# Kernel optimization log

Hardware: AMD Instinct MI355X
Metric: run time of the kernel (lower is better)

## Reference

```python
import jax, jax.numpy as jnp
import numpy as np

TOPK = 13
NUM_CLASSES = 80
ALPHA = 1.0
BETA = 6.0
EPS = 1e-9


def _ciou(gt, pd, eps=1e-7):
    """CIoU between gt (B,M,1,4) and pd (B,1,N,4) xyxy boxes -> (B,M,N)."""
    g_x1, g_y1, g_x2, g_y2 = (gt[..., i] for i in range(4))
    p_x1, p_y1, p_x2, p_y2 = (pd[..., i] for i in range(4))
    iw = jnp.clip(jnp.minimum(g_x2, p_x2) - jnp.maximum(g_x1, p_x1), 0.0)
    ih = jnp.clip(jnp.minimum(g_y2, p_y2) - jnp.maximum(g_y1, p_y1), 0.0)
    inter = iw * ih
    w1, h1 = g_x2 - g_x1, g_y2 - g_y1 + eps
    w2, h2 = p_x2 - p_x1, p_y2 - p_y1 + eps
    union = w1 * h1 + w2 * h2 - inter + eps
    iou = inter / union
    cw = jnp.maximum(g_x2, p_x2) - jnp.minimum(g_x1, p_x1)  # enclosing box
    ch = jnp.maximum(g_y2, p_y2) - jnp.minimum(g_y1, p_y1)
    c2 = cw * cw + ch * ch + eps
    rho2 = ((p_x1 + p_x2 - g_x1 - g_x2) ** 2 + (p_y1 + p_y2 - g_y1 - g_y2) ** 2) / 4.0
    v = (4.0 / jnp.pi ** 2) * (jnp.arctan(w2 / h2) - jnp.arctan(w1 / h1)) ** 2
    a = jax.lax.stop_gradient(v / (v - iou + (1.0 + eps)))  # torch.no_grad alpha
    return iou - (rho2 / c2 + v * a)


def setup_inputs() -> dict:
    key = jax.random.key(0)
    ks = jax.random.split(key, 7)
    B, N, M, C = 16, 8400, 32, NUM_CLASSES
    pd_scores = jax.random.uniform(ks[0], (B, N, C), dtype=jnp.float32)
    # YOLO-style anchor centers for 640x640, strides 8/16/32 -> 8400 points
    pts = []
    for s in (8, 16, 32):
        g = 640 // s
        xs = (jnp.arange(g, dtype=jnp.float32) + 0.5) * s
        xx, yy = jnp.meshgrid(xs, xs, indexing="xy")
        pts.append(jnp.stack([xx.ravel(), yy.ravel()], axis=-1))
    anc_points = jnp.concatenate(pts, axis=0)  # (8400, 2)
    ctr = anc_points[None] + jax.random.normal(ks[1], (B, N, 2)) * 8.0
    wh = jax.random.uniform(ks[2], (B, N, 2), minval=8.0, maxval=128.0)
    pd_bboxes = jnp.concatenate([ctr - wh / 2, ctr + wh / 2], axis=-1)
    gctr = jax.random.uniform(ks[3], (B, M, 2), minval=32.0, maxval=608.0)
    gwh = jax.random.uniform(ks[4], (B, M, 2), minval=16.0, maxval=256.0)
    gt_bboxes = jnp.concatenate([gctr - gwh / 2, gctr + gwh / 2], axis=-1)
    gt_labels = jax.random.randint(ks[5], (B, M, 1), 0, C)
    counts = jax.random.randint(ks[6], (B, 1), 1, M + 1)
    mask_gt = (jnp.arange(M)[None, :] < counts)[..., None]  # (B, M, 1) bool prefix-valid
    return {"pd_scores": pd_scores, "pd_bboxes": pd_bboxes, "anc_points": anc_points,
            "gt_labels": gt_labels, "gt_bboxes": gt_bboxes, "mask_gt": mask_gt}


def reference(pd_scores, pd_bboxes, anc_points, gt_labels, gt_bboxes, mask_gt):
    B, N, C = pd_scores.shape
    M = gt_bboxes.shape[1]
    mask_gt2 = mask_gt[..., 0]  # (B, M) bool
    # --- anchors whose centers lie inside each GT box ---
    lt = gt_bboxes[:, :, None, :2]  # (B, M, 1, 2)
    rb = gt_bboxes[:, :, None, 2:]
    anc = anc_points[None, None]    # (1, 1, N, 2)
    deltas = jnp.concatenate([anc - lt, rb - anc], axis=-1)  # (B, M, N, 4)
    mask_in_gts = jnp.min(deltas, axis=-1) > 1e-9            # (B, M, N)
    valid = mask_in_gts & mask_gt2[:, :, None]
    # --- alignment metric = score^alpha * ciou^beta (masked) ---
    cls = gt_labels[..., 0]                      # (B, M)
    scores_t = jnp.swapaxes(pd_scores, 1, 2)     # (B, C, N)
    bbox_scores = jnp.where(valid, scores_t[jnp.arange(B)[:, None], cls], 0.0)  # (B, M, N)
    overlaps = jnp.where(valid, jnp.clip(_ciou(gt_bboxes[:, :, None], pd_bboxes[:, None]), 0.0), 0.0)
    align_metric = bbox_scores ** ALPHA * overlaps ** BETA
    # --- top-k candidate anchors per GT ---
    _, topk_idx = jax.lax.top_k(align_metric, TOPK)          # (B, M, TOPK)
    bi = jnp.arange(B)[:, None, None]
    mi = jnp.arange(M)[None, :, None]
    src = jnp.broadcast_to(mask_gt2[:, :, None], topk_idx.shape)
    mask_topk = jnp.zeros((B, M, N), dtype=bool).at[bi, mi, topk_idx].set(src)
    mask_pos = mask_topk & valid                             # (B, M, N)
    # --- resolve anchors claimed by multiple GTs: keep highest CIoU ---
    fg_count = jnp.sum(mask_pos, axis=1)                     # (B, N)
    best_gt = jnp.argmax(overlaps, axis=1)                   # (B, N)
    is_max = jnp.arange(M)[None, :, None] == best_gt[:, None, :]
    mask_pos_f = jnp.where(fg_count[:, None, :] > 1, is_max, mask_pos).astype(pd_scores.dtype)
    fg_mask = jnp.sum(mask_pos_f, axis=1)                    # (B, N) float 0/1
    target_gt_idx = jnp.argmax(mask_pos_f, axis=1)           # (B, N)
    # --- gather targets ---
    brow = jnp.arange(B)[:, None]
    target_labels = cls[brow, target_gt_idx]                 # (B, N)
    target_bboxes = gt_bboxes[brow, target_gt_idx]           # (B, N, 4)
    target_scores = jax.nn.one_hot(target_labels, C, dtype=jnp.float32) * fg_mask[..., None]
    # --- normalize scores by per-GT best metric/overlap ---
    align_metric = align_metric * mask_pos_f
    pos_align = jnp.max(align_metric, axis=-1, keepdims=True)            # (B, M, 1)
    pos_over = jnp.max(overlaps * mask_pos_f, axis=-1, keepdims=True)    # (B, M, 1)
    norm_align = jnp.max(align_metric * pos_over / (pos_align + EPS), axis=1)  # (B, N)
    target_scores = target_scores * norm_align[..., None]
    return target_labels, target_bboxes, target_scores, fg_mask > 0, target_gt_idx
```

## Files before the change

### kernel.cpp

```cpp
#include <hip/hip_runtime.h>
#include <math.h>

#define B_ 16
#define N_ 8400
#define M_ 32
#define C_ 80
#define TOPK_ 13
#define KL_ 16
#define MAXC_ 2048
#define MZ_ 4
#define MG_ (M_ / MZ_)

__device__ __forceinline__ bool in_gt(double ax, double ay,
    double gx1, double gy1, double gx2, double gy2) {
  return (ax - gx1 > 1e-9) && (ay - gy1 > 1e-9) &&
         (gx2 - ax > 1e-9) && (gy2 - ay > 1e-9);
}

__device__ __forceinline__ double ciou_ov(
    double px1, double py1, double px2, double py2,
    double gx1, double gy1, double gx2, double gy2,
    double atp, double atg) {
  double iw = fmin(gx2, px2) - fmax(gx1, px1); iw = iw > 0.0 ? iw : 0.0;
  double ih = fmin(gy2, py2) - fmax(gy1, py1); ih = ih > 0.0 ? ih : 0.0;
  double inter = iw * ih;
  double w1 = gx2 - gx1, h1 = gy2 - gy1 + 1e-7;
  double w2 = px2 - px1, h2 = py2 - py1 + 1e-7;
  double uni = w1 * h1 + w2 * h2 - inter + 1e-7;
  double iou = inter / uni;
  double cw = fmax(gx2, px2) - fmin(gx1, px1);
  double ch = fmax(gy2, py2) - fmin(gy1, py1);
  double c2 = cw * cw + ch * ch + 1e-7;
  double dx = px1 + px2 - gx1 - gx2, dy = py1 + py2 - gy1 - gy2;
  double rho2 = (dx * dx + dy * dy) * 0.25;
  double dv = atp - atg;
  double v = (4.0 / (M_PI * M_PI)) * dv * dv;
  double a = v / (v - iou + (1.0 + 1e-7));
  double c = iou - (rho2 / c2 + v * a);
  return c > 0.0 ? c : 0.0;
}

#define MERGE_LISTS(av, ai, bv, bi)                                          \
  {                                                                          \
    _Pragma("unroll")                                                        \
    for (int j = 0; j < KL_; ++j) {                                          \
      double vb = bv[KL_ - 1 - j]; int ib = bi[KL_ - 1 - j];                 \
      bool take = (vb > av[j]) || (vb == av[j] && ib < ai[j]);               \
      av[j] = take ? vb : av[j];                                             \
      ai[j] = take ? ib : ai[j];                                             \
    }                                                                        \
    _Pragma("unroll")                                                        \
    for (int dd = 8; dd >= 1; dd >>= 1) {                                    \
      _Pragma("unroll")                                                      \
      for (int j = 0; j < KL_; ++j) {                                        \
        if (!(j & dd)) {                                                     \
          int kk = j | dd;                                                   \
          bool sw = (av[kk] > av[j]) ||                                      \
                    (av[kk] == av[j] && ai[kk] < ai[j]);                     \
          double xv = av[j]; int xi = ai[j];                                 \
          av[j] = sw ? av[kk] : av[j]; ai[j] = sw ? ai[kk] : ai[j];          \
          av[kk] = sw ? xv : av[kk];   ai[kk] = sw ? xi : ai[kk];            \
        }                                                                    \
      }                                                                      \
    }                                                                        \
  }

__global__ __launch_bounds__(256) void k_prep0(
    const float* __restrict__ gt_bboxes, const unsigned char* __restrict__ raw,
    double* __restrict__ atg, unsigned char* __restrict__ mask,
    unsigned int* __restrict__ MPB, unsigned int* __restrict__ CNT,
    unsigned int* __restrict__ PAL, unsigned int* __restrict__ POV) {
  int gid = blockIdx.x * 256 + threadIdx.x;
  if (gid < B_ * N_) MPB[gid] = 0u;
  if (gid < B_ * M_) {
    double x1 = gt_bboxes[gid * 4 + 0], y1 = gt_bboxes[gid * 4 + 1];
    double x2 = gt_bboxes[gid * 4 + 2], y2 = gt_bboxes[gid * 4 + 3];
    atg[gid] = atan((x2 - x1) / (y2 - y1 + 1e-7));
    CNT[gid] = 0u; PAL[gid] = 0u; POV[gid] = 0u;
  }
  if (blockIdx.x == 0) {
    __shared__ int s_bad;
    int t = threadIdx.x;
    if (t == 0) s_bad = 0;
    __syncthreads();
    if (t < B_) {
      int cnt = 0; bool seen0 = false; bool bad = false;
      for (int m = 0; m < M_; ++m) {
        unsigned char v = raw[t * M_ + m];
        if (v > 1) { bad = true; break; }
        if (v) { if (seen0) { bad = true; break; } ++cnt; }
        else seen0 = true;
      }
      if (cnt < 1) bad = true;
      if (bad) atomicOr(&s_bad, 1);
    }
    __syncthreads();
    bool ok = (s_bad == 0);
    const int* ri = (const int*)raw;
    for (int i = t; i < B_ * M_; i += 256)
      mask[i] = ok ? (raw[i] ? 1 : 0) : ((ri[i] != 0) ? 1 : 0);
  }
}

__global__ __launch_bounds__(256) void k_cand(
    const float* __restrict__ pd_scores, const float* __restrict__ pd_bboxes,
    const float* __restrict__ anc, const int* __restrict__ gt_labels,
    const float* __restrict__ gt_bboxes, const unsigned char* __restrict__ mask,
    const double* __restrict__ atg,
    unsigned int* __restrict__ CNT, double* __restrict__ CV,
    int* __restrict__ CI) {
  int b = blockIdx.y, t = threadIdx.x;
  int m0 = blockIdx.z * MG_;
  int n = blockIdx.x * 256 + t;

  __shared__ double s_g[MG_][4];
  __shared__ double s_atg[MG_];
  __shared__ int s_cls[MG_];
  __shared__ unsigned char s_msk[MG_];
  __shared__ int s_any;
  if (t == 0) s_any = 0;
  __syncthreads();
  if (t < MG_) {
    int row = b * M_ + m0 + t;
    unsigned char mk = mask[row];
    s_msk[t] = mk;
    if (mk) atomicOr(&s_any, 1);
    s_g[t][0] = (double)gt_bboxes[row * 4 + 0];
    s_g[t][1] = (double)gt_bboxes[row * 4 + 1];
    s_g[t][2] = (double)gt_bboxes[row * 4 + 2];
    s_g[t][3] = (double)gt_bboxes[row * 4 + 3];
    s_atg[t] = atg[row];
    s_cls[t] = gt_labels[row];
  }
  __syncthreads();
  if (!s_any) return;
  if (n >= N_) return;

  float2 a2 = ((const float2*)anc)[n];
  double ax = (double)a2.x, ay = (double)a2.y;
  bool have = false;
  double px1 = 0, py1 = 0, px2 = 0, py2 = 0, atpn = 0;
  const float* srow = pd_scores + ((size_t)b * N_ + n) * C_;

  for (int mm = 0; mm < MG_; ++mm) {
    if (!s_msk[mm]) continue;
    double gx1 = s_g[mm][0], gy1 = s_g[mm][1], gx2 = s_g[mm][2], gy2 = s_g[mm][3];
    if (!in_gt(ax, ay, gx1, gy1, gx2, gy2)) continue;
    if (!have) {
      float4 pb = ((const float4*)(pd_bboxes + (size_t)b * N_ * 4))[n];
      px1 = (double)pb.x; py1 = (double)pb.y;
      px2 = (double)pb.z; py2 = (double)pb.w;
      atpn = atan((px2 - px1) / ((py2 - py1) + 1e-7));
      have = true;
    }
    double ov = ciou_ov(px1, py1, px2, py2, gx1, gy1, gx2, gy2, atpn, s_atg[mm]);
    double o2 = ov * ov;
    double am = (double)srow[s_cls[mm]] * (o2 * o2 * o2);
    int row = b * M_ + m0 + mm;
    unsigned int idx = atomicAdd(&CNT[row], 1u);
    if (idx < MAXC_) {
      CV[(size_t)row * MAXC_ + idx] = am;
      CI[(size_t)row * MAXC_ + idx] = n;
    }
  }
}

__global__ __launch_bounds__(256) void k_rowsel(
    const double* __restrict__ CV, const int* __restrict__ CI,
    const unsigned int* __restrict__ CNT,
    const float* __restrict__ anc, const float* __restrict__ gt_bboxes,
    const unsigned char* __restrict__ mask, unsigned int* __restrict__ MPB) {
  int row = blockIdx.x;
  if (!mask[row]) return;
  int b = row >> 5, m = row & 31;
  int t = threadIdx.x;
  int cnt = (int)CNT[row]; if (cnt > MAXC_) cnt = MAXC_;
  const double* cv = CV + (size_t)row * MAXC_;
  const int*    ci = CI + (size_t)row * MAXC_;

  double tv[KL_]; int ti[KL_];
#pragma unroll
  for (int j = 0; j < KL_; ++j) { tv[j] = -1.0; ti[j] = 0x7fffffff; }

  for (int i = t; i < cnt; i += 256) {
    double v = cv[i]; int idx = ci[i];
    if (v > tv[TOPK_ - 1] || (v == tv[TOPK_ - 1] && idx < ti[TOPK_ - 1])) {
      double cvv = v; int cii = idx;
#pragma unroll
      for (int j = 0; j < TOPK_; ++j) {
        bool sw = (cvv > tv[j]) || (cvv == tv[j] && cii < ti[j]);
        double xv = tv[j]; int xi = ti[j];
        if (sw) { tv[j] = cvv; ti[j] = cii; cvv = xv; cii = xi; }
      }
    }
  }

#pragma unroll
  for (int d = 1; d <= 32; d <<= 1) {
    double bv[KL_]; int bi[KL_];
#pragma unroll
    for (int j = 0; j < KL_; ++j) {
      bv[j] = __shfl_xor(tv[j], d, 64);
      bi[j] = __shfl_xor(ti[j], d, 64);
    }
    MERGE_LISTS(tv, ti, bv, bi)
  }

  __shared__ double s_v[4 * KL_];
  __shared__ int    s_i[4 * KL_];
  __shared__ int    s_sel[TOPK_];
  __shared__ int    s_p;
  int wave = t >> 6, lane = t & 63;
  if (lane == 0) {
#pragma unroll
    for (int j = 0; j < KL_; ++j) { s_v[wave * KL_ + j] = tv[j]; s_i[wave * KL_ + j] = ti[j]; }
  }
  __syncthreads();
  if (t == 0) {
    double av[KL_]; int ai[KL_];
#pragma unroll
    for (int j = 0; j < KL_; ++j) { av[j] = s_v[j]; ai[j] = s_i[j]; }
    for (int w = 1; w < 4; ++w) {
      double bv[KL_]; int bi[KL_];
#pragma unroll
      for (int j = 0; j < KL_; ++j) { bv[j] = s_v[w * KL_ + j]; bi[j] = s_i[w * KL_ + j]; }
      MERGE_LISTS(av, ai, bv, bi)
    }
    int p = 0;
#pragma unroll
    for (int j = 0; j < TOPK_; ++j)
      if (av[j] > 0.0) s_sel[p++] = ai[j];
    int nn = 0, slot = p;
    while (slot < TOPK_) {
      bool ispos = false;
      for (int q = 0; q < p; ++q) ispos |= (s_sel[q] == nn);
      if (!ispos) s_sel[slot++] = nn | 0x40000000;
      ++nn;
    }
    s_p = p;
  }
  __syncthreads();

  if (t < TOPK_) {
    int e = s_sel[t];
    if (t < s_p) {
      atomicOr(&MPB[(size_t)b * N_ + e], 1u << m);
    } else {
      int n = e & 0x3fffffff;
      double gx1 = gt_bboxes[row * 4 + 0], gy1 = gt_bboxes[row * 4 + 1];
      double gx2 = gt_bboxes[row * 4 + 2], gy2 = gt_bboxes[row * 4 + 3];
      float2 a2 = ((const float2*)anc)[n];
      if (in_gt((double)a2.x, (double)a2.y, gx1, gy1, gx2, gy2))
        atomicOr(&MPB[(size_t)b * N_ + n], 1u << m);
    }
  }
}

__global__ __launch_bounds__(256) void k_colassign(
    const float* __restrict__ pd_scores, const float* __restrict__ pd_bboxes,
    const float* __restrict__ anc, const int* __restrict__ gt_labels,
    const float* __restrict__ gt_bboxes, const unsigned char* __restrict__ mask,
    const double* __restrict__ atg, const unsigned int* __restrict__ MPB,
    unsigned char* __restrict__ TG, unsigned char* __restrict__ FG,
    float* __restrict__ AMC,
    unsigned int* __restrict__ PAL, unsigned int* __restrict__ POV) {
  int b = blockIdx.y;
  int t = threadIdx.x;
  int n = blockIdx.x * 256 + t;
  int lane = t & 63;
  bool act = (n < N_);

  __shared__ double s_g[M_][4];
  __shared__ double s_atg[M_];
  __shared__ int s_cls[M_];
  __shared__ unsigned char s_msk[M_];
  if (t < M_) {
    int gi = b * M_ + t;
    s_g[t][0] = (double)gt_bboxes[gi * 4 + 0];
    s_g[t][1] = (double)gt_bboxes[gi * 4 + 1];
    s_g[t][2] = (double)gt_bboxes[gi * 4 + 2];
    s_g[t][3] = (double)gt_bboxes[gi * 4 + 3];
    s_atg[t] = atg[gi];
    s_cls[t] = gt_labels[gi];
    s_msk[t] = mask[gi];
  }
  __syncthreads();

  size_t i = (size_t)b * N_ + (act ? n : 0);
  unsigned int mpb = act ? MPB[i] : 0u;
  int cnt = __popc(mpb);

  double ax = 0, ay = 0, px1 = 0, py1 = 0, px2 = 0, py2 = 0;
  if (act && cnt >= 1) {
    float2 a2 = ((const float2*)anc)[n];
    float4 pb = ((const float4*)(pd_bboxes + (size_t)b * N_ * 4))[n];
    ax = (double)a2.x; ay = (double)a2.y;
    px1 = (double)pb.x; py1 = (double)pb.y; px2 = (double)pb.z; py2 = (double)pb.w;
  }

  int tg = 0; unsigned char fg = 0; double ov = 0.0;

  if (act && cnt == 1) {
    fg = 1;
    tg = __ffs(mpb) - 1;
    double atpn = atan((px2 - px1) / ((py2 - py1) + 1e-7));
    double g0 = s_g[tg][0], g1 = s_g[tg][1], g2 = s_g[tg][2], g3 = s_g[tg][3];
    bool val = s_msk[tg] && in_gt(ax, ay, g0, g1, g2, g3);
    ov = val ? ciou_ov(px1, py1, px2, py2, g0, g1, g2, g3, atpn, s_atg[tg]) : 0.0;
  }

  unsigned long long flagged = __ballot(act && cnt > 1);
  while (flagged) {
    int src = __ffsll(flagged) - 1;
    flagged &= flagged - 1;
    double qx  = __shfl(ax, src, 64),  qy  = __shfl(ay, src, 64);
    double q1  = __shfl(px1, src, 64), q2  = __shfl(py1, src, 64);
    double q3  = __shfl(px2, src, 64), q4  = __shfl(py2, src, 64);
    double atq = atan((q3 - q1) / ((q4 - q2) + 1e-7));
    int mm = lane & 31;
    double g0 = s_g[mm][0], g1 = s_g[mm][1], g2 = s_g[mm][2], g3 = s_g[mm][3];
    bool val = s_msk[mm] && in_gt(qx, qy, g0, g1, g2, g3);
    double o = val ? ciou_ov(q1, q2, q3, q4, g0, g1, g2, g3, atq, s_atg[mm]) : 0.0;
    int cm = mm;
#pragma unroll
    for (int d = 1; d < 32; d <<= 1) {
      double oo = __shfl_xor(o, d, 64);
      int    om = __shfl_xor(cm, d, 64);
      if (oo > o || (oo == o && om < cm)) { o = oo; cm = om; }
    }
    if (lane == src) { fg = 1; tg = cm; ov = o; }
  }

  if (!act) return;

  TG[i] = (unsigned char)tg;
  FG[i] = fg;
  if (fg) {
    double o2 = ov * ov;
    double am = (double)pd_scores[i * C_ + s_cls[tg]] * (o2 * o2 * o2);
    float ovf = (float)ov, amf = (float)am;
    AMC[i] = amf;
    atomicMax(&PAL[b * M_ + tg], __float_as_uint(amf));
    atomicMax(&POV[b * M_ + tg], __float_as_uint(ovf));
  }
}

__global__ __launch_bounds__(256) void k_emit(
    const int* __restrict__ gt_labels, const float* __restrict__ gt_bboxes,
    const unsigned char* __restrict__ TG, const unsigned char* __restrict__ FG,
    const float* __restrict__ AMC,
    const unsigned int* __restrict__ PAL, const unsigned int* __restrict__ POV,
    float* __restrict__ out) {
  int b = blockIdx.y;
  int n0 = blockIdx.x * 64;
  int t = threadIdx.x;

  __shared__ float s_g[M_][4];
  __shared__ int s_cls[M_];
  __shared__ float s_pal[M_], s_pov[M_];
  __shared__ float s_na[64];
  __shared__ int   s_lab[64];
  __shared__ int   s_tg[64];
  __shared__ unsigned char s_fg[64];
  if (t < M_) {
    int gi = b * M_ + t;
    s_g[t][0] = gt_bboxes[gi * 4 + 0];
    s_g[t][1] = gt_bboxes[gi * 4 + 1];
    s_g[t][2] = gt_bboxes[gi * 4 + 2];
    s_g[t][3] = gt_bboxes[gi * 4 + 3];
    s_cls[t] = gt_labels[gi];
    s_pal[t] = __uint_as_float(PAL[gi]);
    s_pov[t] = __uint_as_float(POV[gi]);
  }
  __syncthreads();

  if (t < 64) {
    int n = n0 + t;
    if (n < N_) {
      size_t i = (size_t)b * N_ + n;
      int tg = TG[i];
      unsigned char fg = FG[i];
      float na = 0.0f;
      if (fg) {
        double am = (double)AMC[i];
        na = (float)(am * (double)s_pov[tg] / ((double)s_pal[tg] + 1e-9));
      }
      s_na[t] = na; s_lab[t] = s_cls[tg]; s_tg[t] = tg; s_fg[t] = fg;
    }
  }
  __syncthreads();

  float* o0 = out;
  float* o1 = out + (size_t)B_ * N_;
  float* o2 = out + (size_t)B_ * N_ * 5;
  float* o3 = out + (size_t)B_ * N_ * 85;
  float* o4 = out + (size_t)B_ * N_ * 86;

  if (t < 64) {
    int n = n0 + t;
    if (n < N_) {
      size_t i = (size_t)b * N_ + n;
      o0[i] = (float)s_lab[t];
      o3[i] = s_fg[t] ? 1.0f : 0.0f;
      o4[i] = (float)s_tg[t];
      int tg = s_tg[t];
      ((float4*)o1)[i] = make_float4(s_g[tg][0], s_g[tg][1], s_g[tg][2], s_g[tg][3]);
    }
  }

#pragma unroll
  for (int k = 0; k < 5; ++k) {
    int id = t + k * 256;
    int a = id / 20, j = id % 20;
    int n = n0 + a;
    if (n < N_) {
      int lab = s_lab[a];
      float na = s_fg[a] ? s_na[a] : 0.0f;
      int c0 = 4 * j;
      float4 w;
      w.x = (c0 + 0 == lab) ? na : 0.0f;
      w.y = (c0 + 1 == lab) ? na : 0.0f;
      w.z = (c0 + 2 == lab) ? na : 0.0f;
      w.w = (c0 + 3 == lab) ? na : 0.0f;
      ((float4*)(o2 + ((size_t)b * N_ + n) * C_))[j] = w;
    }
  }
}

extern "C" void kernel_launch(void* const* d_in, const int* in_sizes, int n_in,
                              void* d_out, int out_size, void* d_ws, size_t ws_size,
                              hipStream_t stream) {
  const float* pd_scores = (const float*)d_in[0];
  const float* pd_bboxes = (const float*)d_in[1];
  const float* anc       = (const float*)d_in[2];
  const int*   gt_labels = (const int*)d_in[3];
  const float* gt_bboxes = (const float*)d_in[4];
  const unsigned char* mask_raw = (const unsigned char*)d_in[5];

  char* ws = (char*)d_ws;
  size_t off = 0;
  double* CV  = (double*)(ws + off); off += (size_t)B_ * M_ * MAXC_ * 8;
  double* ATG = (double*)(ws + off); off += (size_t)B_ * M_ * 8;
  int*    CI  = (int*)(ws + off);    off += (size_t)B_ * M_ * MAXC_ * 4;
  unsigned int* MPB = (unsigned int*)(ws + off); off += (size_t)B_ * N_ * 4;
  unsigned int* CNT = (unsigned int*)(ws + off); off += (size_t)B_ * M_ * 4;
  unsigned int* PAL = (unsigned int*)(ws + off); off += (size_t)B_ * M_ * 4;
  unsigned int* POV = (unsigned int*)(ws + off); off += (size_t)B_ * M_ * 4;
  unsigned char* TG   = (unsigned char*)(ws + off); off += (size_t)B_ * N_;
  unsigned char* FG   = (unsigned char*)(ws + off); off += (size_t)B_ * N_;
  float* AMC = (float*)(ws + off); off += (size_t)B_ * N_ * 4;
  unsigned char* MASK = (unsigned char*)(ws + off); off += (size_t)B_ * M_;

  k_prep0<<<(B_ * N_ + 255) / 256, 256, 0, stream>>>(gt_bboxes, mask_raw, ATG,
                                                     MASK, MPB, CNT, PAL, POV);
  dim3 gc((N_ + 255) / 256, B_, MZ_);
  k_cand<<<gc, 256, 0, stream>>>(pd_scores, pd_bboxes, anc, gt_labels,
                                 gt_bboxes, MASK, ATG, CNT, CV, CI);
  k_rowsel<<<B_ * M_, 256, 0, stream>>>(CV, CI, CNT, anc, gt_bboxes, MASK, MPB);
  dim3 gbn((N_ + 255) / 256, B_);
  k_colassign<<<gbn, 256, 0, stream>>>(pd_scores, pd_bboxes, anc, gt_labels,
                                       gt_bboxes, MASK, ATG, MPB,
                                       TG, FG, AMC, PAL, POV);
  dim3 gem((N_ + 63) / 64, B_);
  k_emit<<<gem, 256, 0, stream>>>(gt_labels, gt_bboxes, TG, FG, AMC, PAL, POV,
                                  (float*)d_out);
}
```

Baseline: 162.5 us.

## Shrink prep kernel, recompute atan in place, wave-per-row topk, emit outputs in colassign

The prep kernel shrinks to two blocks. The MPB zeroing moves into the candidate kernel, and the per-GT atan is recomputed in shared-memory setup instead of being stored to a workspace array. Row top-k selection now uses one wavefront per GT row with four rows per block, which removes the cross-wave shared-memory merge and the barriers. Label, bbox, fg and index outputs are written directly in the column-assign kernel, so the final kernel only writes the score tensor. Together these cut the size of the prep launch, workspace traffic and block synchronisation. The costs are redundant atan work per block and a single wave scanning each candidate list.

```diff
diff --git a/kernel.cpp b/kernel.cpp
--- a/kernel.cpp
+++ b/kernel.cpp
@@ -66,18 +66,11 @@
   }
 
 __global__ __launch_bounds__(256) void k_prep0(
-    const float* __restrict__ gt_bboxes, const unsigned char* __restrict__ raw,
-    double* __restrict__ atg, unsigned char* __restrict__ mask,
-    unsigned int* __restrict__ MPB, unsigned int* __restrict__ CNT,
+    const unsigned char* __restrict__ raw, unsigned char* __restrict__ mask,
+    unsigned int* __restrict__ CNT,
     unsigned int* __restrict__ PAL, unsigned int* __restrict__ POV) {
   int gid = blockIdx.x * 256 + threadIdx.x;
-  if (gid < B_ * N_) MPB[gid] = 0u;
-  if (gid < B_ * M_) {
-    double x1 = gt_bboxes[gid * 4 + 0], y1 = gt_bboxes[gid * 4 + 1];
-    double x2 = gt_bboxes[gid * 4 + 2], y2 = gt_bboxes[gid * 4 + 3];
-    atg[gid] = atan((x2 - x1) / (y2 - y1 + 1e-7));
-    CNT[gid] = 0u; PAL[gid] = 0u; POV[gid] = 0u;
-  }
+  if (gid < B_ * M_) { CNT[gid] = 0u; PAL[gid] = 0u; POV[gid] = 0u; }
   if (blockIdx.x == 0) {
     __shared__ int s_bad;
     int t = threadIdx.x;
@@ -106,12 +99,14 @@
     const float* __restrict__ pd_scores, const float* __restrict__ pd_bboxes,
     const float* __restrict__ anc, const int* __restrict__ gt_labels,
     const float* __restrict__ gt_bboxes, const unsigned char* __restrict__ mask,
-    const double* __restrict__ atg,
+    unsigned int* __restrict__ MPB,
     unsigned int* __restrict__ CNT, double* __restrict__ CV,
     int* __restrict__ CI) {
   int b = blockIdx.y, t = threadIdx.x;
   int m0 = blockIdx.z * MG_;
   int n = blockIdx.x * 256 + t;
+
+  if (blockIdx.z == 0 && n < N_) MPB[(size_t)b * N_ + n] = 0u;
 
   __shared__ double s_g[MG_][4];
   __shared__ double s_atg[MG_];
@@ -125,11 +120,10 @@
     unsigned char mk = mask[row];
     s_msk[t] = mk;
     if (mk) atomicOr(&s_any, 1);
-    s_g[t][0] = (double)gt_bboxes[row * 4 + 0];
-    s_g[t][1] = (double)gt_bboxes[row * 4 + 1];
-    s_g[t][2] = (double)gt_bboxes[row * 4 + 2];
-    s_g[t][3] = (double)gt_bboxes[row * 4 + 3];
-    s_atg[t] = atg[row];
+    double x1 = (double)gt_bboxes[row * 4 + 0], y1 = (double)gt_bboxes[row * 4 + 1];
+    double x2 = (double)gt_bboxes[row * 4 + 2], y2 = (double)gt_bboxes[row * 4 + 3];
+    s_g[t][0] = x1; s_g[t][1] = y1; s_g[t][2] = x2; s_g[t][3] = y2;
+    s_atg[t] = atan((x2 - x1) / (y2 - y1 + 1e-7));
     s_cls[t] = gt_labels[row];
   }
   __syncthreads();
@@ -170,10 +164,11 @@
     const unsigned int* __restrict__ CNT,
     const float* __restrict__ anc, const float* __restrict__ gt_bboxes,
     const unsigned char* __restrict__ mask, unsigned int* __restrict__ MPB) {
-  int row = blockIdx.x;
-  if (!mask[row]) return;
+  int t = threadIdx.x;
+  int lane = t & 63;
+  int row = blockIdx.x * 4 + (t >> 6);
+  if (row >= B_ * M_ || !mask[row]) return;
   int b = row >> 5, m = row & 31;
-  int t = threadIdx.x;
   int cnt = (int)CNT[row]; if (cnt > MAXC_) cnt = MAXC_;
   const double* cv = CV + (size_t)row * MAXC_;
   const int*    ci = CI + (size_t)row * MAXC_;
@@ -182,7 +177,7 @@
 #pragma unroll
   for (int j = 0; j < KL_; ++j) { tv[j] = -1.0; ti[j] = 0x7fffffff; }
 
-  for (int i = t; i < cnt; i += 256) {
+  for (int i = lane; i < cnt; i += 64) {
     double v = cv[i]; int idx = ci[i];
     if (v > tv[TOPK_ - 1] || (v == tv[TOPK_ - 1] && idx < ti[TOPK_ - 1])) {
       double cvv = v; int cii = idx;
@@ -206,47 +201,38 @@
     MERGE_LISTS(tv, ti, bv, bi)
   }
 
-  __shared__ double s_v[4 * KL_];
-  __shared__ int    s_i[4 * KL_];
-  __shared__ int    s_sel[TOPK_];
-  __shared__ int    s_p;
-  int wave = t >> 6, lane = t & 63;
+  int sel[TOPK_]; int p = 0;
   if (lane == 0) {
 #pragma unroll
-    for (int j = 0; j < KL_; ++j) { s_v[wave * KL_ + j] = tv[j]; s_i[wave * KL_ + j] = ti[j]; }
-  }
-  __syncthreads();
-  if (t == 0) {
-    double av[KL_]; int ai[KL_];
-#pragma unroll
-    for (int j = 0; j < KL_; ++j) { av[j] = s_v[j]; ai[j] = s_i[j]; }
-    for (int w = 1; w < 4; ++w) {
-      double bv[KL_]; int bi[KL_];
-#pragma unroll
-      for (int j = 0; j < KL_; ++j) { bv[j] = s_v[w * KL_ + j]; bi[j] = s_i[w * KL_ + j]; }
-      MERGE_LISTS(av, ai, bv, bi)
-    }
-    int p = 0;
+    for (int j = 0; j < TOPK_; ++j) sel[j] = -1;
 #pragma unroll
     for (int j = 0; j < TOPK_; ++j)
-      if (av[j] > 0.0) s_sel[p++] = ai[j];
+      if (tv[j] > 0.0) sel[p++] = ti[j];
     int nn = 0, slot = p;
     while (slot < TOPK_) {
       bool ispos = false;
-      for (int q = 0; q < p; ++q) ispos |= (s_sel[q] == nn);
-      if (!ispos) s_sel[slot++] = nn | 0x40000000;
+#pragma unroll
+      for (int q = 0; q < TOPK_; ++q) ispos |= (q < p && sel[q] == nn);
+      if (!ispos) { 
+#pragma unroll
+        for (int q = 0; q < TOPK_; ++q) if (q == slot) sel[q] = nn | 0x40000000;
+        ++slot;
+      }
       ++nn;
     }
-    s_p = p;
-  }
-  __syncthreads();
-
-  if (t < TOPK_) {
-    int e = s_sel[t];
-    if (t < s_p) {
-      atomicOr(&MPB[(size_t)b * N_ + e], 1u << m);
+  }
+  int pbc = __shfl(p, 0, 64);
+  int mine = -1;
+#pragma unroll
+  for (int j = 0; j < TOPK_; ++j) {
+    int v = __shfl(sel[j], 0, 64);
+    if (lane == j) mine = v;
+  }
+  if (lane < TOPK_) {
+    if (lane < pbc) {
+      atomicOr(&MPB[(size_t)b * N_ + mine], 1u << m);
     } else {
-      int n = e & 0x3fffffff;
+      int n = mine & 0x3fffffff;
       double gx1 = gt_bboxes[row * 4 + 0], gy1 = gt_bboxes[row * 4 + 1];
       double gx2 = gt_bboxes[row * 4 + 2], gy2 = gt_bboxes[row * 4 + 3];
       float2 a2 = ((const float2*)anc)[n];
@@ -260,10 +246,11 @@
     const float* __restrict__ pd_scores, const float* __restrict__ pd_bboxes,
     const float* __restrict__ anc, const int* __restrict__ gt_labels,
     const float* __restrict__ gt_bboxes, const unsigned char* __restrict__ mask,
-    const double* __restrict__ atg, const unsigned int* __restrict__ MPB,
+    const unsigned int* __restrict__ MPB,
     unsigned char* __restrict__ TG, unsigned char* __restrict__ FG,
     float* __restrict__ AMC,
-    unsigned int* __restrict__ PAL, unsigned int* __restrict__ POV) {
+    unsigned int* __restrict__ PAL, unsigned int* __restrict__ POV,
+    float* __restrict__ out) {
   int b = blockIdx.y;
   int t = threadIdx.x;
   int n = blockIdx.x * 256 + t;
@@ -276,11 +263,10 @@
   __shared__ unsigned char s_msk[M_];
   if (t < M_) {
     int gi = b * M_ + t;
-    s_g[t][0] = (double)gt_bboxes[gi * 4 + 0];
-    s_g[t][1] = (double)gt_bboxes[gi * 4 + 1];
-    s_g[t][2] = (double)gt_bboxes[gi * 4 + 2];
-    s_g[t][3] = (double)gt_bboxes[gi * 4 + 3];
-    s_atg[t] = atg[gi];
+    double x1 = (double)gt_bboxes[gi * 4 + 0], y1 = (double)gt_bboxes[gi * 4 + 1];
+    double x2 = (double)gt_bboxes[gi * 4 + 2], y2 = (double)gt_bboxes[gi * 4 + 3];
+    s_g[t][0] = x1; s_g[t][1] = y1; s_g[t][2] = x2; s_g[t][3] = y2;
+    s_atg[t] = atan((x2 - x1) / (y2 - y1 + 1e-7));
     s_cls[t] = gt_labels[gi];
     s_msk[t] = mask[gi];
   }
@@ -343,10 +329,20 @@
     atomicMax(&PAL[b * M_ + tg], __float_as_uint(amf));
     atomicMax(&POV[b * M_ + tg], __float_as_uint(ovf));
   }
-}
-
-__global__ __launch_bounds__(256) void k_emit(
-    const int* __restrict__ gt_labels, const float* __restrict__ gt_bboxes,
+
+  float* o0 = out;
+  float* o1 = out + (size_t)B_ * N_;
+  float* o3 = out + (size_t)B_ * N_ * 85;
+  float* o4 = out + (size_t)B_ * N_ * 86;
+  o0[i] = (float)s_cls[tg];
+  o3[i] = fg ? 1.0f : 0.0f;
+  o4[i] = (float)tg;
+  ((float4*)o1)[i] = make_float4((float)s_g[tg][0], (float)s_g[tg][1],
+                                 (float)s_g[tg][2], (float)s_g[tg][3]);
+}
+
+__global__ __launch_bounds__(256) void k_sc(
+    const int* __restrict__ gt_labels,
     const unsigned char* __restrict__ TG, const unsigned char* __restrict__ FG,
     const float* __restrict__ AMC,
     const unsigned int* __restrict__ PAL, const unsigned int* __restrict__ POV,
@@ -355,19 +351,12 @@
   int n0 = blockIdx.x * 64;
   int t = threadIdx.x;
 
-  __shared__ float s_g[M_][4];
   __shared__ int s_cls[M_];
   __shared__ float s_pal[M_], s_pov[M_];
   __shared__ float s_na[64];
   __shared__ int   s_lab[64];
-  __shared__ int   s_tg[64];
-  __shared__ unsigned char s_fg[64];
   if (t < M_) {
     int gi = b * M_ + t;
-    s_g[t][0] = gt_bboxes[gi * 4 + 0];
-    s_g[t][1] = gt_bboxes[gi * 4 + 1];
-    s_g[t][2] = gt_bboxes[gi * 4 + 2];
-    s_g[t][3] = gt_bboxes[gi * 4 + 3];
     s_cls[t] = gt_labels[gi];
     s_pal[t] = __uint_as_float(PAL[gi]);
     s_pov[t] = __uint_as_float(POV[gi]);
@@ -379,35 +368,17 @@
     if (n < N_) {
       size_t i = (size_t)b * N_ + n;
       int tg = TG[i];
-      unsigned char fg = FG[i];
       float na = 0.0f;
-      if (fg) {
+      if (FG[i]) {
         double am = (double)AMC[i];
         na = (float)(am * (double)s_pov[tg] / ((double)s_pal[tg] + 1e-9));
       }
-      s_na[t] = na; s_lab[t] = s_cls[tg]; s_tg[t] = tg; s_fg[t] = fg;
+      s_na[t] = na; s_lab[t] = s_cls[tg];
     }
   }
   __syncthreads();
 
-  float* o0 = out;
-  float* o1 = out + (size_t)B_ * N_;
   float* o2 = out + (size_t)B_ * N_ * 5;
-  float* o3 = out + (size_t)B_ * N_ * 85;
-  float* o4 = out + (size_t)B_ * N_ * 86;
-
-  if (t < 64) {
-    int n = n0 + t;
-    if (n < N_) {
-      size_t i = (size_t)b * N_ + n;
-      o0[i] = (float)s_lab[t];
-      o3[i] = s_fg[t] ? 1.0f : 0.0f;
-      o4[i] = (float)s_tg[t];
-      int tg = s_tg[t];
-      ((float4*)o1)[i] = make_float4(s_g[tg][0], s_g[tg][1], s_g[tg][2], s_g[tg][3]);
-    }
-  }
-
 #pragma unroll
   for (int k = 0; k < 5; ++k) {
     int id = t + k * 256;
@@ -415,7 +386,7 @@
     int n = n0 + a;
     if (n < N_) {
       int lab = s_lab[a];
-      float na = s_fg[a] ? s_na[a] : 0.0f;
+      float na = s_na[a];
       int c0 = 4 * j;
       float4 w;
       w.x = (c0 + 0 == lab) ? na : 0.0f;
@@ -440,7 +411,6 @@
   char* ws = (char*)d_ws;
   size_t off = 0;
   double* CV  = (double*)(ws + off); off += (size_t)B_ * M_ * MAXC_ * 8;
-  double* ATG = (double*)(ws + off); off += (size_t)B_ * M_ * 8;
   int*    CI  = (int*)(ws + off);    off += (size_t)B_ * M_ * MAXC_ * 4;
   unsigned int* MPB = (unsigned int*)(ws + off); off += (size_t)B_ * N_ * 4;
   unsigned int* CNT = (unsigned int*)(ws + off); off += (size_t)B_ * M_ * 4;
@@ -451,17 +421,17 @@
   float* AMC = (float*)(ws + off); off += (size_t)B_ * N_ * 4;
   unsigned char* MASK = (unsigned char*)(ws + off); off += (size_t)B_ * M_;
 
-  k_prep0<<<(B_ * N_ + 255) / 256, 256, 0, stream>>>(gt_bboxes, mask_raw, ATG,
-                                                     MASK, MPB, CNT, PAL, POV);
+  k_prep0<<<2, 256, 0, stream>>>(mask_raw, MASK, CNT, PAL, POV);
   dim3 gc((N_ + 255) / 256, B_, MZ_);
   k_cand<<<gc, 256, 0, stream>>>(pd_scores, pd_bboxes, anc, gt_labels,
-                                 gt_bboxes, MASK, ATG, CNT, CV, CI);
-  k_rowsel<<<B_ * M_, 256, 0, stream>>>(CV, CI, CNT, anc, gt_bboxes, MASK, MPB);
+                                 gt_bboxes, MASK, MPB, CNT, CV, CI);
+  k_rowsel<<<(B_ * M_ + 3) / 4, 256, 0, stream>>>(CV, CI, CNT, anc, gt_bboxes,
+                                                  MASK, MPB);
   dim3 gbn((N_ + 255) / 256, B_);
   k_colassign<<<gbn, 256, 0, stream>>>(pd_scores, pd_bboxes, anc, gt_labels,
-                                       gt_bboxes, MASK, ATG, MPB,
-                                       TG, FG, AMC, PAL, POV);
-  dim3 gem((N_ + 63) / 64, B_);
-  k_emit<<<gem, 256, 0, stream>>>(gt_labels, gt_bboxes, TG, FG, AMC, PAL, POV,
-                                  (float*)d_out);
-}
+                                       gt_bboxes, MASK, MPB,
+                                       TG, FG, AMC, PAL, POV, (float*)d_out);
+  dim3 gsc((N_ + 63) / 64, B_);
+  k_sc<<<gsc, 256, 0, stream>>>(gt_labels, TG, FG, AMC, PAL, POV,
+                                (float*)d_out);
+}
```

New measurement: 167.5 us. +3.1%, slower.
